# Optimization experiments

Measured on AMD Instinct MI355X. Metric: run time of the kernel, lower is better.

Reference implementation:

```python
import jax, jax.numpy as jnp
import numpy as np

H = 16          # num heads
DH = 64         # head dim
D = H * DH      # hidden = 1024


def setup_inputs() -> dict:
    key = jax.random.key(0)
    ks = jax.random.split(key, 9)
    s = 1.0 / np.sqrt(D)
    return {
        "hidden_states": jax.random.normal(ks[0], (4, 2048, D), dtype=jnp.float32),
        "Wq": jax.random.normal(ks[1], (D, D), dtype=jnp.float32) * s,
        "bq": jax.random.normal(ks[2], (D,), dtype=jnp.float32) * 0.02,
        "Wk": jax.random.normal(ks[3], (D, D), dtype=jnp.float32) * s,
        "bk": jax.random.normal(ks[4], (D,), dtype=jnp.float32) * 0.02,
        "Wv": jax.random.normal(ks[5], (D, D), dtype=jnp.float32) * s,
        "bv": jax.random.normal(ks[6], (D,), dtype=jnp.float32) * 0.02,
        "Wo": jax.random.normal(ks[7], (D, D), dtype=jnp.float32) * s,
        "bo": jax.random.normal(ks[8], (D,), dtype=jnp.float32) * 0.02,
    }


def _split_heads(x):  # [B,S,D] -> [B,H,S,DH]
    B, S, _ = x.shape
    return x.reshape(B, S, H, DH).transpose(0, 2, 1, 3)


def reference(hidden_states, Wq, bq, Wk, bk, Wv, bv, Wo, bo):
    # torch Linear: y = x @ W.T + b  (W stored as [out, in])
    q = _split_heads(jnp.einsum('bsd,ed->bse', hidden_states, Wq) + bq)
    k = _split_heads(jnp.einsum('bsd,ed->bse', hidden_states, Wk) + bk)
    v = _split_heads(jnp.einsum('bsd,ed->bse', hidden_states, Wv) + bv)
    scores = jnp.einsum('bhqd,bhkd->bhqk', q, k) / np.sqrt(DH)
    probs = jax.nn.softmax(scores, axis=-1)  # fused softmax+matmul in original
    ctx = jnp.einsum('bhqk,bhkd->bhqd', probs, v)
    B, _, S, _ = ctx.shape
    ctx = ctx.transpose(0, 2, 1, 3).reshape(B, S, D)
    out = jnp.einsum('bsd,ed->bse', ctx, Wo) + bo
    return out  # weights are None (vis=False); dropout rate asserted 0
```

## Files before the change

kernel.cpp:

```cpp
#include <hip/hip_runtime.h>


typedef __bf16 bf16;
typedef __bf16 bf16x8 __attribute__((ext_vector_type(8)));
typedef __bf16 bf16x4 __attribute__((ext_vector_type(4)));
typedef float  floatx4 __attribute__((ext_vector_type(4)));

#define NB   4
#define SEQ  2048
#define NH   16
#define DH   64
#define DIM  1024
#define MTOT (NB * SEQ)

#define CEXP 0.18033688f

__device__ __forceinline__ floatx4 zero4() {
    floatx4 z; z[0] = 0.f; z[1] = 0.f; z[2] = 0.f; z[3] = 0.f; return z;
}

__device__ __forceinline__ void load_lds16(const bf16* g, bf16* l) {
    __builtin_amdgcn_global_load_lds(
        (__attribute__((address_space(1))) void*)g,
        (__attribute__((address_space(3))) void*)l,
        16, 0, 0);
}

__global__ __launch_bounds__(256) void cvt_all(const float* __restrict__ X,
                                               const float* __restrict__ w0,
                                               const float* __restrict__ w1,
                                               const float* __restrict__ w2,
                                               const float* __restrict__ w3,
                                               bf16* __restrict__ Xb,
                                               bf16* __restrict__ Wb) {
    const size_t MD = (size_t)MTOT * DIM;
    const size_t DD = (size_t)DIM * DIM;
    size_t i = ((size_t)blockIdx.x * 256 + threadIdx.x) * 4;
    float4 f; bf16* dst;
    if (i < MD) {
        f = *(const float4*)(X + i);
        dst = Xb + i;
    } else {
        size_t off = i - MD;
        int w = (int)(off >> 20);
        size_t wi = off & (DD - 1);
        const float* ws = (w == 0) ? w0 : (w == 1) ? w1 : (w == 2) ? w2 : w3;
        f = *(const float4*)(ws + wi);
        dst = Wb + off;
    }
    bf16x4 o;
    o[0] = (bf16)f.x; o[1] = (bf16)f.y; o[2] = (bf16)f.z; o[3] = (bf16)f.w;
    *(bf16x4*)dst = o;
}

__global__ __launch_bounds__(256) void gemm_qkv(const bf16* __restrict__ A,
                                                const bf16* __restrict__ W,
                                                const float* __restrict__ bq,
                                                const float* __restrict__ bk,
                                                const float* __restrict__ bv,
                                                bf16* __restrict__ Qo,
                                                bf16* __restrict__ Ko,
                                                bf16* __restrict__ Vt) {
    __shared__ __align__(16) bf16 As[128 * 32];
    __shared__ __align__(16) bf16 Bs[128 * 32];
    __shared__ __align__(16) bf16 Ts[64 * 136];

    const int tid  = threadIdx.x;
    const int wave = tid >> 6, lane = tid & 63;
    const int quad = lane >> 4, l16 = lane & 15;
    const int sel = blockIdx.x >> 3;
    const int nt  = blockIdx.x & 7;
    const int m0 = blockIdx.y * 128, n0 = nt * 128;
    const int wm = (wave & 1) * 64, wn = (wave >> 1) * 64;
    const bf16* Wsel = W + (size_t)(sel * DIM + n0) * DIM;
    const float* bias = (sel == 0) ? bq : (sel == 1) ? bk : bv;
    const float scale = (sel == 0) ? CEXP : 1.0f;

    floatx4 acc[4][4];
#pragma unroll
    for (int mi = 0; mi < 4; mi++)
#pragma unroll
        for (int ni = 0; ni < 4; ni++) acc[mi][ni] = zero4();

    for (int k0 = 0; k0 < DIM; k0 += 32) {
        __syncthreads();
#pragma unroll
        for (int i = 0; i < 2; i++) {
            const int cb = wave * 128 + i * 64;
            const int c  = cb + lane;
            const int row = c >> 2;
            const int kc  = (c & 3) * 8;
            load_lds16(A + (size_t)(m0 + row) * DIM + k0 + kc, &As[cb * 8]);
            load_lds16(Wsel + (size_t)row * DIM + k0 + kc, &Bs[cb * 8]);
        }
        __syncthreads();

        bf16x8 af[4], bfr[4];
#pragma unroll
        for (int mi = 0; mi < 4; mi++)
            af[mi] = *(const bf16x8*)&As[(wm + mi * 16 + l16) * 32 + quad * 8];
#pragma unroll
        for (int ni = 0; ni < 4; ni++)
            bfr[ni] = *(const bf16x8*)&Bs[(wn + ni * 16 + l16) * 32 + quad * 8];
#pragma unroll
        for (int mi = 0; mi < 4; mi++)
#pragma unroll
            for (int ni = 0; ni < 4; ni++)
                acc[mi][ni] = __builtin_amdgcn_mfma_f32_16x16x32_bf16(
                    af[mi], bfr[ni], acc[mi][ni], 0, 0, 0);
    }

    if (sel < 2) {
        bf16* C = (sel == 0) ? Qo : Ko;
#pragma unroll
        for (int mi = 0; mi < 4; mi++) {
            const int rbase = m0 + wm + mi * 16 + quad * 4;
#pragma unroll
            for (int ni = 0; ni < 4; ni++) {
                const int col = n0 + wn + ni * 16 + l16;
                const float bval = bias[col];
#pragma unroll
                for (int i = 0; i < 4; i++)
                    C[(size_t)(rbase + i) * DIM + col] =
                        (bf16)((acc[mi][ni][i] + bval) * scale);
            }
        }
    } else {
        const int b  = blockIdx.y >> 4;
        const int s0 = (blockIdx.y & 15) * 128;
#pragma unroll
        for (int r = 0; r < 2; r++) {
            __syncthreads();
            if ((wave >> 1) == r) {
#pragma unroll
                for (int mi = 0; mi < 4; mi++) {
                    const int m_l = wm + mi * 16 + quad * 4;
#pragma unroll
                    for (int ni = 0; ni < 4; ni++) {
                        const int n_loc = ni * 16 + l16;
                        const float bval = bias[n0 + 64 * r + n_loc];
#pragma unroll
                        for (int i = 0; i < 4; i++)
                            Ts[n_loc * 136 + m_l + i] = (bf16)(acc[mi][ni][i] + bval);
                    }
                }
            }
            __syncthreads();
            const int hh = 2 * nt + r;
            bf16* obase = Vt + ((size_t)(b * NH + hh) * DH) * SEQ + s0;
#pragma unroll
            for (int p = 0; p < 4; p++) {
                const int chunk = p * 256 + tid;
                const int row = chunk >> 4, c0 = (chunk & 15) * 8;
                bf16x8 v = *(const bf16x8*)&Ts[row * 136 + c0];
                *(bf16x8*)(obase + (size_t)row * SEQ + c0) = v;
            }
        }
    }
}

__global__ __launch_bounds__(256) void gemm_out(const bf16* __restrict__ A,
                                                const bf16* __restrict__ W,
                                                const float* __restrict__ bias,
                                                float* __restrict__ C) {
    __shared__ __align__(16) bf16 As[128 * 32];
    __shared__ __align__(16) bf16 Bs[128 * 32];

    const int tid  = threadIdx.x;
    const int wave = tid >> 6, lane = tid & 63;
    const int quad = lane >> 4, l16 = lane & 15;
    const int m0 = blockIdx.y * 128, n0 = blockIdx.x * 128;
    const int wm = (wave & 1) * 64, wn = (wave >> 1) * 64;

    floatx4 acc[4][4];
#pragma unroll
    for (int mi = 0; mi < 4; mi++)
#pragma unroll
        for (int ni = 0; ni < 4; ni++) acc[mi][ni] = zero4();

    for (int k0 = 0; k0 < DIM; k0 += 32) {
        __syncthreads();
#pragma unroll
        for (int i = 0; i < 2; i++) {
            const int cb = wave * 128 + i * 64;
            const int c  = cb + lane;
            const int row = c >> 2;
            const int kc  = (c & 3) * 8;
            load_lds16(A + (size_t)(m0 + row) * DIM + k0 + kc, &As[cb * 8]);
            load_lds16(W + (size_t)(n0 + row) * DIM + k0 + kc, &Bs[cb * 8]);
        }
        __syncthreads();

        bf16x8 af[4], bfr[4];
#pragma unroll
        for (int mi = 0; mi < 4; mi++)
            af[mi] = *(const bf16x8*)&As[(wm + mi * 16 + l16) * 32 + quad * 8];
#pragma unroll
        for (int ni = 0; ni < 4; ni++)
            bfr[ni] = *(const bf16x8*)&Bs[(wn + ni * 16 + l16) * 32 + quad * 8];
#pragma unroll
        for (int mi = 0; mi < 4; mi++)
#pragma unroll
            for (int ni = 0; ni < 4; ni++)
                acc[mi][ni] = __builtin_amdgcn_mfma_f32_16x16x32_bf16(
                    af[mi], bfr[ni], acc[mi][ni], 0, 0, 0);
    }

#pragma unroll
    for (int mi = 0; mi < 4; mi++) {
        const int rbase = m0 + wm + mi * 16 + quad * 4;
#pragma unroll
        for (int ni = 0; ni < 4; ni++) {
            const int col = n0 + wn + ni * 16 + l16;
            const float bval = bias[col];
#pragma unroll
            for (int i = 0; i < 4; i++)
                C[(size_t)(rbase + i) * DIM + col] = acc[mi][ni][i] + bval;
        }
    }
}

__global__ __launch_bounds__(256, 4) void attn_kernel(const bf16* __restrict__ Q,
                                                      const bf16* __restrict__ K,
                                                      const bf16* __restrict__ Vt,
                                                      bf16* __restrict__ Ctx) {
    __shared__ __align__(16) bf16 Ks[2][64 * 64];
    __shared__ __align__(16) bf16 Vs[2][64 * 64];

    const int tid  = threadIdx.x;
    const int wave = tid >> 6, lane = tid & 63;
    const int quad = lane >> 4, l16 = lane & 15;
    const int xcd = blockIdx.x & 7;
    const int j   = blockIdx.x >> 3;
    const int bh  = xcd * 8 + (j >> 4);
    const int qb  = j & 15;
    const int b   = bh >> 4, h = bh & 15;

    const size_t base_bh = (size_t)b * SEQ * DIM + (size_t)h * DH;
    const size_t base_v  = (size_t)bh * DH * SEQ;
    const int qt = qb * 128 + wave * 32;

    bf16x8 aq[2][2];
#pragma unroll
    for (int m = 0; m < 2; m++) {
        const bf16* qp = Q + base_bh + (size_t)(qt + m * 16 + l16) * DIM + quad * 8;
        aq[m][0] = *(const bf16x8*)qp;
        aq[m][1] = *(const bf16x8*)(qp + 32);
    }

    const int sc = wave * 128 + lane;
    int srow[2], scol[2];
    srow[0] = sc >> 3;        srow[1] = (sc + 64) >> 3;
    scol[0] = (sc & 7) ^ (srow[0] & 7);
    scol[1] = ((sc + 64) & 7) ^ (srow[1] & 7);
    auto kvloc = [](int r) {
        const int w = r >> 5, rw = r & 31, r4 = rw & 15;
        return w * 32 + ((rw >> 4) << 2) + ((r4 >> 2) << 3) + (r4 & 3);
    };
    const bf16* kga = K + base_bh + (size_t)kvloc(srow[0]) * DIM + scol[0] * 8;
    const bf16* kgb = K + base_bh + (size_t)kvloc(srow[1]) * DIM + scol[1] * 8;
    const bf16* vga = Vt + base_v + (size_t)srow[0] * SEQ + scol[0] * 8;
    const bf16* vgb = Vt + base_v + (size_t)srow[1] * SEQ + scol[1] * 8;
    const int ldsa = (wave * 128) * 8, ldsb = (wave * 128 + 64) * 8;

    int koa[4], kob[4], vo[2][4];
#pragma unroll
    for (int g = 0; g < 4; g++) {
        const int krow = g * 16 + l16;
        koa[g] = (krow * 8 + (quad ^ (krow & 7))) * 8;
        kob[g] = (krow * 8 + ((4 + quad) ^ (krow & 7))) * 8;
    }
#pragma unroll
    for (int w = 0; w < 2; w++)
#pragma unroll
        for (int dt = 0; dt < 4; dt++) {
            const int d = dt * 16 + l16;
            vo[w][dt] = d * 64 + ((4 * w + quad) ^ (d & 7)) * 8;
        }

    bf16x8 ones8;
#pragma unroll
    for (int i = 0; i < 8; i++) ones8[i] = (bf16)1.0f;

    floatx4 acc[2][4], accl[2];
#pragma unroll
    for (int m = 0; m < 2; m++) {
        accl[m] = zero4();
#pragma unroll
        for (int dt = 0; dt < 4; dt++) acc[m][dt] = zero4();
    }

    load_lds16(kga, &Ks[0][ldsa]);
    load_lds16(kgb, &Ks[0][ldsb]);
    load_lds16(vga, &Vs[0][ldsa]);
    load_lds16(vgb, &Vs[0][ldsb]);

    for (int it = 0; it < SEQ / 64; it++) {
        __syncthreads();
        const int cur = it & 1;
        if (it + 1 < SEQ / 64) {
            const int nxt = cur ^ 1;
            const size_t kvn = (size_t)(it + 1) * 64;
            load_lds16(kga + kvn * DIM, &Ks[nxt][ldsa]);
            load_lds16(kgb + kvn * DIM, &Ks[nxt][ldsb]);
            load_lds16(vga + kvn, &Vs[nxt][ldsa]);
            load_lds16(vgb + kvn, &Vs[nxt][ldsb]);
        }

#pragma unroll
        for (int w = 0; w < 2; w++) {
            const bf16x8 ke0 = *(const bf16x8*)&Ks[cur][koa[2 * w]];
            const bf16x8 ke1 = *(const bf16x8*)&Ks[cur][kob[2 * w]];
            const bf16x8 ko0 = *(const bf16x8*)&Ks[cur][koa[2 * w + 1]];
            const bf16x8 ko1 = *(const bf16x8*)&Ks[cur][kob[2 * w + 1]];
            bf16x8 pw[2];
#pragma unroll
            for (int m = 0; m < 2; m++) {
                floatx4 sa = zero4(), sb = zero4();
                sa = __builtin_amdgcn_mfma_f32_16x16x32_bf16(ke0, aq[m][0], sa, 0, 0, 0);
                sa = __builtin_amdgcn_mfma_f32_16x16x32_bf16(ke1, aq[m][1], sa, 0, 0, 0);
                sb = __builtin_amdgcn_mfma_f32_16x16x32_bf16(ko0, aq[m][0], sb, 0, 0, 0);
                sb = __builtin_amdgcn_mfma_f32_16x16x32_bf16(ko1, aq[m][1], sb, 0, 0, 0);
                bf16x8 p;
#pragma unroll
                for (int i = 0; i < 4; i++) {
                    p[i]     = (bf16)__builtin_amdgcn_exp2f(sa[i]);
                    p[4 + i] = (bf16)__builtin_amdgcn_exp2f(sb[i]);
                }
                pw[m] = p;
            }
            bf16x8 vf[4];
#pragma unroll
            for (int dt = 0; dt < 4; dt++)
                vf[dt] = *(const bf16x8*)&Vs[cur][vo[w][dt]];
#pragma unroll
            for (int m = 0; m < 2; m++) {
#pragma unroll
                for (int dt = 0; dt < 4; dt++)
                    acc[m][dt] = __builtin_amdgcn_mfma_f32_16x16x32_bf16(
                        pw[m], vf[dt], acc[m][dt], 0, 0, 0);
                accl[m] = __builtin_amdgcn_mfma_f32_16x16x32_bf16(
                    pw[m], ones8, accl[m], 0, 0, 0);
            }
        }
    }

#pragma unroll
    for (int m = 0; m < 2; m++) {
        float inv[4];
#pragma unroll
        for (int i = 0; i < 4; i++) inv[i] = 1.0f / accl[m][i];
        bf16* cp = Ctx + base_bh + (size_t)(qt + m * 16 + quad * 4) * DIM + l16;
#pragma unroll
        for (int i = 0; i < 4; i++)
#pragma unroll
            for (int dt = 0; dt < 4; dt++)
                cp[(size_t)i * DIM + dt * 16] = (bf16)(acc[m][dt][i] * inv[i]);
    }
}

extern "C" void kernel_launch(void* const* d_in, const int* in_sizes, int n_in,
                              void* d_out, int out_size, void* d_ws, size_t ws_size,
                              hipStream_t stream) {
    const float* X  = (const float*)d_in[0];
    const float* Wq = (const float*)d_in[1];
    const float* bq = (const float*)d_in[2];
    const float* Wk = (const float*)d_in[3];
    const float* bk = (const float*)d_in[4];
    const float* Wv = (const float*)d_in[5];
    const float* bv = (const float*)d_in[6];
    const float* Wo = (const float*)d_in[7];
    const float* bo = (const float*)d_in[8];
    float* out = (float*)d_out;

    const size_t MD = (size_t)MTOT * DIM;
    const size_t DD = (size_t)DIM * DIM;

    bf16* Xb  = (bf16*)d_ws;
    bf16* Qb  = Xb + MD;
    bf16* Kb  = Qb + MD;
    bf16* Vtb = Kb + MD;
    bf16* Wqb = Vtb + MD;
    bf16* Wob = Wqb + 3 * DD;
    if (ws_size < (MD * 4 + DD * 4) * sizeof(bf16)) return;

    cvt_all<<<(int)((MD + 4 * DD) / 4 / 256), 256, 0, stream>>>(
        X, Wq, Wk, Wv, Wo, Xb, Wqb);

    gemm_qkv<<<dim3(24, MTOT / 128), 256, 0, stream>>>(Xb, Wqb, bq, bk, bv,
                                                       Qb, Kb, Vtb);

    attn_kernel<<<NB * NH * (SEQ / 128), 256, 0, stream>>>(Qb, Kb, Vtb, Xb);

    gemm_out<<<dim3(8, MTOT / 128), 256, 0, stream>>>(Xb, Wob, bo, out);
}
```

Baseline: 280.9 us.

## Rewrite QKV GEMM with 256x256 tiles, 4-stage LDS pipeline and swizzle

The QKV projection GEMM moves from 128x128 tiles with 4 waves and single-buffered LDS to 256x256 tiles with 8 waves and a 4-deep ring of LDS stages. Global-to-LDS loads for future k-tiles are interleaved with MFMA work, using explicit vmcnt waits, raw barriers and setprio. LDS rows use an XOR swizzle to avoid bank conflicts, and blocks are remapped so that tiles sharing inputs run close together in time for L2 reuse. The V-transpose epilogue is rewritten over the larger tile with a swizzled layout. The cost is much higher register and LDS pressure (128KB LDS per block) and hand-tuned wait counts that could be fragile.

New measurement: 271.6 us. 1.03x faster.

```diff
diff --git a/kernel.cpp b/kernel.cpp
--- a/kernel.cpp
+++ b/kernel.cpp
@@ -53,108 +53,168 @@
     *(bf16x4*)dst = o;
 }
 
-__global__ __launch_bounds__(256) void gemm_qkv(const bf16* __restrict__ A,
-                                                const bf16* __restrict__ W,
-                                                const float* __restrict__ bq,
-                                                const float* __restrict__ bk,
-                                                const float* __restrict__ bv,
-                                                bf16* __restrict__ Qo,
-                                                bf16* __restrict__ Ko,
-                                                bf16* __restrict__ Vt) {
-    __shared__ __align__(16) bf16 As[128 * 32];
-    __shared__ __align__(16) bf16 Bs[128 * 32];
-    __shared__ __align__(16) bf16 Ts[64 * 136];
+#define QKV_TILE(T_, DO_STAGE_, WAITSTR_) do {                                 \
+    const int bsel_ = (T_) & 3;                                                \
+    const bf16* bA_ = smem + bsel_ * 16384;                                    \
+    const bf16* bB_ = bA_ + 8192;                                              \
+    bf16* sA_ = smem + (((T_) + 3) & 3) * 16384;                               \
+    bf16* sB_ = sA_ + 8192;                                                    \
+    const int ko_ = ((T_) + 3) * 32;                                           \
+    bf16x8 afr_[4], bfg_[4];                                                   \
+    _Pragma("unroll")                                                          \
+    for (int mf = 0; mf < 4; mf++) afr_[mf] = *(const bf16x8*)(bA_ + aoff[mf]);\
+    _Pragma("unroll")                                                          \
+    for (int nf = 0; nf < 4; nf++) bfg_[nf] = *(const bf16x8*)(bB_ + boff[nf]);\
+    if (DO_STAGE_) {                                                           \
+        load_lds16(gA0 + ko_, sA_ + soff0);                                    \
+        load_lds16(gA1 + ko_, sA_ + soff1);                                    \
+    }                                                                          \
+    __builtin_amdgcn_s_barrier();                                              \
+    __builtin_amdgcn_s_setprio(1);                                             \
+    _Pragma("unroll")                                                          \
+    for (int mf = 0; mf < 4; mf++)                                             \
+        _Pragma("unroll")                                                      \
+        for (int nf = 0; nf < 4; nf++)                                         \
+            acc[mf][nf] = __builtin_amdgcn_mfma_f32_16x16x32_bf16(             \
+                afr_[mf], bfg_[nf], acc[mf][nf], 0, 0, 0);                     \
+    __builtin_amdgcn_s_setprio(0);                                             \
+    __builtin_amdgcn_s_barrier();                                              \
+    _Pragma("unroll")                                                          \
+    for (int mf = 0; mf < 4; mf++)                                             \
+        afr_[mf] = *(const bf16x8*)(bA_ + aoff[4 + mf]);                       \
+    if (DO_STAGE_) {                                                           \
+        load_lds16(gB0 + ko_, sB_ + soff0);                                    \
+        load_lds16(gB1 + ko_, sB_ + soff1);                                    \
+    }                                                                          \
+    __builtin_amdgcn_s_barrier();                                              \
+    __builtin_amdgcn_s_setprio(1);                                             \
+    _Pragma("unroll")                                                          \
+    for (int mf = 0; mf < 4; mf++)                                             \
+        _Pragma("unroll")                                                      \
+        for (int nf = 0; nf < 4; nf++)                                         \
+            acc[4 + mf][nf] = __builtin_amdgcn_mfma_f32_16x16x32_bf16(         \
+                afr_[mf], bfg_[nf], acc[4 + mf][nf], 0, 0, 0);                 \
+    __builtin_amdgcn_s_setprio(0);                                             \
+    asm volatile(WAITSTR_ ::: "memory");                                       \
+    __builtin_amdgcn_s_barrier();                                              \
+} while (0)
+
+__global__ __launch_bounds__(512, 2) void gemm_qkv(const bf16* __restrict__ A,
+                                                   const bf16* __restrict__ W,
+                                                   const float* __restrict__ bq,
+                                                   const float* __restrict__ bk,
+                                                   const float* __restrict__ bv,
+                                                   bf16* __restrict__ Qo,
+                                                   bf16* __restrict__ Ko,
+                                                   bf16* __restrict__ Vt) {
+    __shared__ __align__(16) bf16 smem[4 * 16384];
 
     const int tid  = threadIdx.x;
     const int wave = tid >> 6, lane = tid & 63;
     const int quad = lane >> 4, l16 = lane & 15;
-    const int sel = blockIdx.x >> 3;
-    const int nt  = blockIdx.x & 7;
-    const int m0 = blockIdx.y * 128, n0 = nt * 128;
-    const int wm = (wave & 1) * 64, wn = (wave >> 1) * 64;
+    const int wr = wave >> 2, wc = wave & 3;
+
+    const int wg = (blockIdx.x & 7) * 48 + (blockIdx.x >> 3);
+    const int mt = wg / 12, inner = wg % 12;
+    const int sel = inner >> 2, nt = inner & 3;
+    const int m0 = mt * 256, n0 = nt * 256;
+
     const bf16* Wsel = W + (size_t)(sel * DIM + n0) * DIM;
     const float* bias = (sel == 0) ? bq : (sel == 1) ? bk : bv;
-    const float scale = (sel == 0) ? CEXP : 1.0f;
-
-    floatx4 acc[4][4];
-#pragma unroll
-    for (int mi = 0; mi < 4; mi++)
-#pragma unroll
-        for (int ni = 0; ni < 4; ni++) acc[mi][ni] = zero4();
-
-    for (int k0 = 0; k0 < DIM; k0 += 32) {
-        __syncthreads();
-#pragma unroll
-        for (int i = 0; i < 2; i++) {
-            const int cb = wave * 128 + i * 64;
-            const int c  = cb + lane;
-            const int row = c >> 2;
-            const int kc  = (c & 3) * 8;
-            load_lds16(A + (size_t)(m0 + row) * DIM + k0 + kc, &As[cb * 8]);
-            load_lds16(Wsel + (size_t)row * DIM + k0 + kc, &Bs[cb * 8]);
-        }
-        __syncthreads();
-
-        bf16x8 af[4], bfr[4];
-#pragma unroll
-        for (int mi = 0; mi < 4; mi++)
-            af[mi] = *(const bf16x8*)&As[(wm + mi * 16 + l16) * 32 + quad * 8];
-#pragma unroll
-        for (int ni = 0; ni < 4; ni++)
-            bfr[ni] = *(const bf16x8*)&Bs[(wn + ni * 16 + l16) * 32 + quad * 8];
-#pragma unroll
-        for (int mi = 0; mi < 4; mi++)
-#pragma unroll
-            for (int ni = 0; ni < 4; ni++)
-                acc[mi][ni] = __builtin_amdgcn_mfma_f32_16x16x32_bf16(
-                    af[mi], bfr[ni], acc[mi][ni], 0, 0, 0);
-    }
+
+    int aoff[8], boff[4];
+#pragma unroll
+    for (int mf = 0; mf < 8; mf++) {
+        const int row = wr * 128 + mf * 16 + l16;
+        aoff[mf] = row * 32 + ((quad ^ ((row >> 1) & 3)) * 8);
+    }
+#pragma unroll
+    for (int nf = 0; nf < 4; nf++) {
+        const int row = wc * 64 + nf * 16 + l16;
+        boff[nf] = row * 32 + ((quad ^ ((row >> 1) & 3)) * 8);
+    }
+
+    const int c0 = tid, c1 = tid + 512;
+    const int ra0 = c0 >> 2, qa0 = (c0 & 3) ^ ((ra0 >> 1) & 3);
+    const int ra1 = c1 >> 2, qa1 = (c1 & 3) ^ ((ra1 >> 1) & 3);
+    const bf16* gA0 = A + (size_t)(m0 + ra0) * DIM + qa0 * 8;
+    const bf16* gA1 = A + (size_t)(m0 + ra1) * DIM + qa1 * 8;
+    const bf16* gB0 = Wsel + (size_t)ra0 * DIM + qa0 * 8;
+    const bf16* gB1 = Wsel + (size_t)ra1 * DIM + qa1 * 8;
+    const int soff0 = (wave * 64) * 8;
+    const int soff1 = (512 + wave * 64) * 8;
+
+    floatx4 acc[8][4];
+#pragma unroll
+    for (int mf = 0; mf < 8; mf++)
+#pragma unroll
+        for (int nf = 0; nf < 4; nf++) acc[mf][nf] = zero4();
+
+#pragma unroll
+    for (int kt = 0; kt < 3; kt++) {
+        bf16* sA = smem + kt * 16384;
+        bf16* sB = sA + 8192;
+        load_lds16(gA0 + kt * 32, sA + soff0);
+        load_lds16(gA1 + kt * 32, sA + soff1);
+        load_lds16(gB0 + kt * 32, sB + soff0);
+        load_lds16(gB1 + kt * 32, sB + soff1);
+    }
+    asm volatile("s_waitcnt vmcnt(8)" ::: "memory");
+    __builtin_amdgcn_s_barrier();
+
+    const int NT = DIM / 32;
+#pragma unroll 1
+    for (int t = 0; t < NT - 3; t++)
+        QKV_TILE(t, true, "s_waitcnt vmcnt(8)");
+    QKV_TILE(NT - 3, false, "s_waitcnt vmcnt(4)");
+    QKV_TILE(NT - 2, false, "s_waitcnt vmcnt(0)");
+    QKV_TILE(NT - 1, false, "s_waitcnt vmcnt(0)");
 
     if (sel < 2) {
         bf16* C = (sel == 0) ? Qo : Ko;
-#pragma unroll
-        for (int mi = 0; mi < 4; mi++) {
-            const int rbase = m0 + wm + mi * 16 + quad * 4;
-#pragma unroll
-            for (int ni = 0; ni < 4; ni++) {
-                const int col = n0 + wn + ni * 16 + l16;
+        const float scale = (sel == 0) ? CEXP : 1.0f;
+#pragma unroll
+        for (int mf = 0; mf < 8; mf++) {
+            const int rbase = m0 + wr * 128 + mf * 16 + quad * 4;
+#pragma unroll
+            for (int nf = 0; nf < 4; nf++) {
+                const int col = n0 + wc * 64 + nf * 16 + l16;
                 const float bval = bias[col];
 #pragma unroll
                 for (int i = 0; i < 4; i++)
                     C[(size_t)(rbase + i) * DIM + col] =
-                        (bf16)((acc[mi][ni][i] + bval) * scale);
+                        (bf16)((acc[mf][nf][i] + bval) * scale);
             }
         }
     } else {
-        const int b  = blockIdx.y >> 4;
-        const int s0 = (blockIdx.y & 15) * 128;
-#pragma unroll
-        for (int r = 0; r < 2; r++) {
-            __syncthreads();
-            if ((wave >> 1) == r) {
-#pragma unroll
-                for (int mi = 0; mi < 4; mi++) {
-                    const int m_l = wm + mi * 16 + quad * 4;
-#pragma unroll
-                    for (int ni = 0; ni < 4; ni++) {
-                        const int n_loc = ni * 16 + l16;
-                        const float bval = bias[n0 + 64 * r + n_loc];
-#pragma unroll
-                        for (int i = 0; i < 4; i++)
-                            Ts[n_loc * 136 + m_l + i] = (bf16)(acc[mi][ni][i] + bval);
-                    }
-                }
+        const int b  = m0 >> 11;
+        const int s0 = m0 & (SEQ - 1);
+#pragma unroll
+        for (int mf = 0; mf < 8; mf++) {
+            const int mb = wr * 128 + mf * 16 + quad * 4;
+#pragma unroll
+            for (int nf = 0; nf < 4; nf++) {
+                const int n_loc = wc * 64 + nf * 16 + l16;
+                const float bval = bias[n0 + n_loc];
+                bf16x4 pk;
+#pragma unroll
+                for (int i = 0; i < 4; i++) pk[i] = (bf16)(acc[mf][nf][i] + bval);
+                const int e = n_loc * 256 + (((mb * 2) ^ ((n_loc & 7) << 4)) >> 1);
+                *(bf16x4*)(smem + e) = pk;
             }
-            __syncthreads();
-            const int hh = 2 * nt + r;
-            bf16* obase = Vt + ((size_t)(b * NH + hh) * DH) * SEQ + s0;
-#pragma unroll
-            for (int p = 0; p < 4; p++) {
-                const int chunk = p * 256 + tid;
-                const int row = chunk >> 4, c0 = (chunk & 15) * 8;
-                bf16x8 v = *(const bf16x8*)&Ts[row * 136 + c0];
-                *(bf16x8*)(obase + (size_t)row * SEQ + c0) = v;
-            }
+        }
+        asm volatile("s_waitcnt lgkmcnt(0)" ::: "memory");
+        __builtin_amdgcn_s_barrier();
+#pragma unroll
+        for (int p = 0; p < 16; p++) {
+            const int c = p * 512 + tid;
+            const int n_loc = c >> 5, mc = (c & 31) * 8;
+            const int e = n_loc * 256 + (((mc * 2) ^ ((n_loc & 7) << 4)) >> 1);
+            bf16x8 v = *(const bf16x8*)(smem + e);
+            const int dg = n0 + n_loc;
+            const int hh = dg >> 6, d = dg & 63;
+            bf16* op = Vt + ((size_t)(b * NH + hh) * DH + d) * SEQ + s0 + mc;
+            *(bf16x8*)op = v;
         }
     }
 }
@@ -387,8 +447,7 @@
     cvt_all<<<(int)((MD + 4 * DD) / 4 / 256), 256, 0, stream>>>(
         X, Wq, Wk, Wv, Wo, Xb, Wqb);
 
-    gemm_qkv<<<dim3(24, MTOT / 128), 256, 0, stream>>>(Xb, Wqb, bq, bk, bv,
-                                                       Qb, Kb, Vtb);
+    gemm_qkv<<<384, 512, 0, stream>>>(Xb, Wqb, bq, bk, bv, Qb, Kb, Vtb);
 
     attn_kernel<<<NB * NH * (SEQ / 128), 256, 0, stream>>>(Qb, Kb, Vtb, Xb);
 
```
